# Kernel optimization log

Measured on AMD Instinct MI355X. Metric: run time of the kernel, lower is better.

Reference implementation:

```python
import jax, jax.numpy as jnp
import numpy as np

TOP_K = 2
SCALING = 16.0 / 8.0  # alpha / rank


def setup_inputs() -> dict:
    key = jax.random.key(0)
    ks = jax.random.split(key, 9)
    B, V, D, P = 32, 21, 512, 64
    IN, OUT, E, R, H = D * P, 96, 8, 8, 256
    return {
        "x": jax.random.normal(ks[0], (B, V, D, P), jnp.float32),
        "W_base": jax.random.normal(ks[1], (OUT, IN), jnp.float32) * (IN ** -0.5),
        "b_base": jax.random.normal(ks[2], (OUT,), jnp.float32) * 0.01,
        "W1": jax.random.normal(ks[3], (H, D), jnp.float32) * (D ** -0.5),
        "b1": jax.random.normal(ks[4], (H,), jnp.float32) * 0.01,
        "W2": jax.random.normal(ks[5], (E, H), jnp.float32) * (H ** -0.5),
        "b2": jax.random.normal(ks[6], (E,), jnp.float32) * 0.01,
        "lora_A": jax.random.normal(ks[7], (E, R, IN), jnp.float32) * (IN ** -0.5),
        "lora_B": jax.random.normal(ks[8], (E, OUT, R), jnp.float32) * (R ** -0.5),
    }


def reference(x, W_base, b_base, W1, b1, W2, b2, lora_A, lora_B):
    B, V, D, P = x.shape
    E = lora_A.shape[0]
    # FlattenHead: flatten last two dims, then linear (dropout is identity in eval)
    flat = x.reshape(B, V, D * P)                      # [B, V, IN]
    base_out = flat @ W_base.T + b_base                # [B, V, OUT]
    # Router: pool over n_vars then patch dim -> [B, D]
    pooled = x.mean(axis=1).mean(axis=-1)
    h = jax.nn.relu(pooled @ W1.T + b1)
    logits = h @ W2.T + b2                             # [B, E]
    probs = jax.nn.softmax(logits, axis=-1)
    topw, topi = jax.lax.top_k(probs, TOP_K)           # [B, K]
    topw = topw / jnp.clip(topw.sum(-1, keepdims=True), 1e-6)
    # All LoRA experts (matches original dense compute), then weighted combine
    temp = jnp.einsum("bvi,eri->ebvr", flat, lora_A)   # [E, B, V, R]
    delta = jnp.einsum("ebvr,eor->ebvo", temp, lora_B) * SCALING  # [E, B, V, OUT]
    # Scatter top-k weights into dense [B, E] then combine (top-k sparse combine)
    w_full = jnp.zeros((B, E), x.dtype).at[jnp.arange(B)[:, None], topi].add(topw)
    moe_delta = jnp.einsum("be,ebvo->bvo", w_full, delta)
    return base_out + moe_delta, probs
```

## Files before the change

kernel.cpp:

```cpp
#include <hip/hip_runtime.h>

#define B_DIM 32
#define V_DIM 21
#define D_DIM 512
#define P_DIM 64
#define M_TOTAL 672
#define K_TOTAL 32768
#define OUT_DIM 96
#define E_DIM 8
#define R_DIM 8
#define H_DIM 256
#define N_TOTAL 160
#define SCALING 2.0f
#define POOL_SCALE (1.0f / (V_DIM * (float)P_DIM))

#define BM 64
#define BK 32
#define KSPLIT 32
#define K_PER_SPLIT (K_TOTAL / KSPLIT)
#define CHUNKS (K_PER_SPLIT / BK)
#define SMN (M_TOTAL * N_TOTAL)
#define NMB 11
#define RC_ROWS 4

typedef __attribute__((ext_vector_type(4))) float floatx4;
typedef __attribute__((ext_vector_type(8))) short short8;
typedef __attribute__((ext_vector_type(2))) unsigned int uintx2;

__device__ __forceinline__ unsigned int cvt_pk_bf16(float lo, float hi) {
  unsigned int r;
  asm("v_cvt_pk_bf16_f32 %0, %1, %2" : "=v"(r) : "v"(lo), "v"(hi));
  return r;
}

__device__ __forceinline__ void gl_lds16(const void* g, void* l) {
  __builtin_amdgcn_global_load_lds(
      (const __attribute__((address_space(1))) void*)g,
      (__attribute__((address_space(3))) void*)l, 16, 0, 0);
}

__global__ __launch_bounds__(256, 4)
void gemm_kernel(const float* __restrict__ x, const float* __restrict__ W_base,
                 const float* __restrict__ lora_A, float* __restrict__ P,
                 float* __restrict__ pp) {
  __shared__ __attribute__((aligned(16))) float ldsA[2][BM * BK];
  __shared__ __attribute__((aligned(16))) short ldsB[2][N_TOTAL * BK];
  __shared__ float lds_pool[5 * 16];

  const int tid = threadIdx.x;
  const int mb = blockIdx.x;
  const int m0 = mb * BM;
  const int ky = blockIdx.y;
  const int kbase = ky * K_PER_SPLIT;
  const int lane = tid & 63;
  const int wave = tid >> 6;
  const int quad = lane >> 4;
  const int l16 = lane & 15;
  const int b_first = m0 / V_DIM;
  const int d_first = ky * (K_PER_SPLIT / P_DIM);

  if (tid < 80) lds_pool[tid] = 0.0f;

  const float* srcA[2]; int dstA[2];
  #pragma unroll
  for (int it = 0; it < 2; ++it) {
    int idx = it * 256 + tid;
    int row = idx >> 3, j = idx & 7;
    int m = m0 + row; if (m > M_TOTAL - 1) m = M_TOTAL - 1;
    srcA[it] = x + (size_t)m * K_TOTAL + kbase + ((j ^ (row & 7)) << 2);
    dstA[it] = (it * 256 + (tid & 192)) << 2;
  }

  const float* srcB[5]; int offB[5];
  #pragma unroll
  for (int it = 0; it < 5; ++it) {
    int idx = it * 256 + tid;
    int row = idx >> 3, j = idx & 7;
    const float* wrow = (row < OUT_DIM)
        ? (W_base + (size_t)row * K_TOTAL)
        : (lora_A + (size_t)(row - OUT_DIM) * K_TOTAL);
    srcB[it] = wrow + kbase + (j << 2);
    int p = row >> 1;
    int c8 = ((row & 1) << 2) | (j >> 1);
    offB[it] = p * 64 + ((c8 ^ (p & 7)) << 3) + ((j & 1) << 2);
  }

  const int prow = tid >> 2;
  const int part = tid & 3;
  const int ps1 = (prow + part) & 7;
  const int ps2 = (ps1 + 4) & 7;
  const int pm = m0 + prow;
  const int pool_base = (pm < M_TOTAL) ? ((pm / V_DIM) - b_first) * 16 : -1;

  floatx4 rb[5];
  floatx4 acc[10];
  #pragma unroll
  for (int nt = 0; nt < 10; ++nt) acc[nt] = (floatx4)(0.0f);

#define BLOAD(c)                                                              \
  { _Pragma("unroll")                                                         \
    for (int it = 0; it < 5; ++it)                                            \
      rb[it] = *(const floatx4*)(srcB[it] + (c) * BK); }
#define AISSUE(c, bb)                                                         \
  { _Pragma("unroll")                                                         \
    for (int it = 0; it < 2; ++it)                                            \
      gl_lds16(srcA[it] + (c) * BK, &ldsA[bb][dstA[it]]); }
#define BWRITE(bb)                                                            \
  { _Pragma("unroll")                                                         \
    for (int it = 0; it < 5; ++it) {                                          \
      uintx2 w;                                                               \
      w[0] = cvt_pk_bf16(rb[it][0], rb[it][1]);                               \
      w[1] = cvt_pk_bf16(rb[it][2], rb[it][3]);                               \
      *(uintx2*)&ldsB[bb][offB[it]] = w;                                      \
    } }

  BLOAD(0); AISSUE(0, 0); BWRITE(0);
  __syncthreads();

  #pragma unroll 2
  for (int c = 0; c < CHUNKS; ++c) {
    const int buf = c & 1;
    if (c + 1 < CHUNKS) { BLOAD(c + 1); AISSUE(c + 1, buf ^ 1); }
    {
      const floatx4* aT = (const floatx4*)ldsA[buf];
      floatx4 u = aT[prow * 8 + ps1];
      floatx4 w = aT[prow * 8 + ps2];
      float s = ((u[0] + u[1]) + (u[2] + u[3])) + ((w[0] + w[1]) + (w[2] + w[3]));
      s += __shfl_down(s, 2, 4);
      s += __shfl_down(s, 1, 4);
      if (part == 0 && pool_base >= 0)
        atomicAdd(&lds_pool[pool_base + (c >> 1)], s);
    }
    {
      const floatx4* aT = (const floatx4*)ldsA[buf];
      const int r = wave * 16 + l16;
      floatx4 f0 = aT[r * 8 + ((2 * quad) ^ (r & 7))];
      floatx4 f1 = aT[r * 8 + ((2 * quad + 1) ^ (r & 7))];
      union { short8 s; unsigned int u[4]; } av;
      av.u[0] = cvt_pk_bf16(f0[0], f0[1]);
      av.u[1] = cvt_pk_bf16(f0[2], f0[3]);
      av.u[2] = cvt_pk_bf16(f1[0], f1[1]);
      av.u[3] = cvt_pk_bf16(f1[2], f1[3]);
      const short8* bT = (const short8*)ldsB[buf];
      #pragma unroll
      for (int nt = 0; nt < 10; ++nt) {
        int r2 = nt * 16 + l16;
        int pr = r2 >> 1;
        short8 b = bT[pr * 8 + ((((r2 & 1) << 2) | quad) ^ (pr & 7))];
        acc[nt] = __builtin_amdgcn_mfma_f32_16x16x32_bf16(av.s, b, acc[nt], 0, 0, 0);
      }
    }
    if (c + 1 < CHUNKS) BWRITE(buf ^ 1);
    __syncthreads();
  }

  {
    const int mrow = m0 + wave * 16 + quad * 4;
    float* Pp = P + (size_t)ky * SMN + (size_t)mrow * N_TOTAL + l16;
    #pragma unroll
    for (int r = 0; r < 4; ++r)
      if (mrow + r < M_TOTAL)
        #pragma unroll
        for (int nt = 0; nt < 10; ++nt)
          Pp[(size_t)r * N_TOTAL + nt * 16] = acc[nt][r];
  }

  if (tid < 80) {
    int bl = tid >> 4, dl = tid & 15;
    pp[((size_t)(mb * 5 + bl)) * D_DIM + d_first + dl] = lds_pool[tid];
  }
}

__global__ __launch_bounds__(256)
void router_kernel(const float* __restrict__ pp, const float* __restrict__ W1,
                   const float* __restrict__ b1, const float* __restrict__ W2,
                   const float* __restrict__ b2, float* __restrict__ wfull,
                   float* __restrict__ probs_out) {
  __shared__ float sp[D_DIM];
  __shared__ float sh[H_DIM];
  __shared__ float slog[E_DIM];
  const int b = blockIdx.x;
  const int t = threadIdx.x;
  const int mb1 = (b * V_DIM) / BM;
  const int mb2 = (b * V_DIM + V_DIM - 1) / BM;
  const int bf1 = (mb1 * BM) / V_DIM;
  const int bf2 = (mb2 * BM) / V_DIM;
  const float* p1 = pp + (size_t)(mb1 * 5 + (b - bf1)) * D_DIM;
  const float* p2 = pp + (size_t)(mb2 * 5 + (b - bf2)) * D_DIM;
  for (int d = t; d < D_DIM; d += 256) {
    float v = p1[d];
    if (mb2 != mb1) v += p2[d];
    sp[d] = v * POOL_SCALE;
  }
  __syncthreads();
  float acc = b1[t];
  const float* w1r = W1 + (size_t)t * D_DIM;
  for (int d = 0; d < D_DIM; ++d) acc += sp[d] * w1r[d];
  sh[t] = fmaxf(acc, 0.0f);
  __syncthreads();
  if (t < E_DIM) {
    float a = b2[t];
    const float* w2r = W2 + t * H_DIM;
    for (int j = 0; j < H_DIM; ++j) a += sh[j] * w2r[j];
    slog[t] = a;
  }
  __syncthreads();
  if (t == 0) {
    float p[E_DIM];
    float mx = slog[0];
    for (int e = 1; e < E_DIM; ++e) mx = fmaxf(mx, slog[e]);
    float se = 0.0f;
    for (int e = 0; e < E_DIM; ++e) { p[e] = __expf(slog[e] - mx); se += p[e]; }
    float inv = 1.0f / se;
    for (int e = 0; e < E_DIM; ++e) { p[e] *= inv; probs_out[b * E_DIM + e] = p[e]; }
    int i0 = 0;
    for (int e = 1; e < E_DIM; ++e) if (p[e] > p[i0]) i0 = e;
    int i1 = (i0 == 0) ? 1 : 0;
    for (int e = 0; e < E_DIM; ++e) if (e != i0 && p[e] > p[i1]) i1 = e;
    float s2 = p[i0] + p[i1];
    float invs = 1.0f / fmaxf(s2, 1e-6f);
    for (int e = 0; e < E_DIM; ++e) {
      float w = 0.0f;
      if (e == i0) w += p[i0] * invs;
      if (e == i1) w += p[i1] * invs;
      wfull[b * E_DIM + e] = w;
    }
  }
}

__global__ __launch_bounds__(256)
void reduce_combine_kernel(const float* __restrict__ P, const float* __restrict__ b_base,
                           const float* __restrict__ lora_B, const float* __restrict__ wfull,
                           float* __restrict__ out) {
  __shared__ float sS[RC_ROWS * N_TOTAL];
  const int t = threadIdx.x;
  const int NF4 = RC_ROWS * N_TOTAL / 4;
  if (t < NF4) {
    const floatx4* P4 = (const floatx4*)P;
    size_t base = (size_t)blockIdx.x * NF4 + t;
    floatx4 a = (floatx4)(0.0f);
    #pragma unroll 8
    for (int k = 0; k < KSPLIT; ++k) a += P4[(size_t)k * (SMN / 4) + base];
    *(floatx4*)&sS[t * 4] = a;
  }
  __syncthreads();
  for (int i = t; i < RC_ROWS * OUT_DIM; i += 256) {
    int mr = i / OUT_DIM;
    int o = i - mr * OUT_DIM;
    int mm = blockIdx.x * RC_ROWS + mr;
    int b = mm / V_DIM;
    const float* srow = sS + mr * N_TOTAL;
    float res = srow[o] + b_base[o];
    float moe = 0.0f;
    #pragma unroll
    for (int e = 0; e < E_DIM; ++e) {
      float we = wfull[b * E_DIM + e];
      if (we != 0.0f) {
        const float* lb = lora_B + ((size_t)e * OUT_DIM + o) * R_DIM;
        float dd = 0.0f;
        #pragma unroll
        for (int r = 0; r < R_DIM; ++r) dd += srow[OUT_DIM + e * R_DIM + r] * lb[r];
        moe += we * dd;
      }
    }
    out[(size_t)mm * OUT_DIM + o] = res + SCALING * moe;
  }
}

extern "C" void kernel_launch(void* const* d_in, const int* in_sizes, int n_in,
                              void* d_out, int out_size, void* d_ws, size_t ws_size,
                              hipStream_t stream) {
  const float* x      = (const float*)d_in[0];
  const float* W_base = (const float*)d_in[1];
  const float* b_base = (const float*)d_in[2];
  const float* W1     = (const float*)d_in[3];
  const float* b1     = (const float*)d_in[4];
  const float* W2     = (const float*)d_in[5];
  const float* b2     = (const float*)d_in[6];
  const float* lora_A = (const float*)d_in[7];
  const float* lora_B = (const float*)d_in[8];
  float* out = (float*)d_out;

  float* ws    = (float*)d_ws;
  float* pp    = ws;
  float* wfull = ws + NMB * 5 * D_DIM;
  float* P     = wfull + 256;

  gemm_kernel<<<dim3(NMB, KSPLIT), 256, 0, stream>>>(x, W_base, lora_A, P, pp);
  router_kernel<<<B_DIM, 256, 0, stream>>>(pp, W1, b1, W2, b2, wfull,
                                           out + (size_t)M_TOTAL * OUT_DIM);
  reduce_combine_kernel<<<M_TOTAL / RC_ROWS, 256, 0, stream>>>(
      P, b_base, lora_B, wfull, out);
}
```

Measured before the change: 216.9 us.

## Pre-convert weights to bf16 and use 4-stage async LDS pipeline

```diff
diff --git a/kernel.cpp b/kernel.cpp
--- a/kernel.cpp
+++ b/kernel.cpp
@@ -25,7 +25,12 @@
 
 typedef __attribute__((ext_vector_type(4))) float floatx4;
 typedef __attribute__((ext_vector_type(8))) short short8;
-typedef __attribute__((ext_vector_type(2))) unsigned int uintx2;
+
+__device__ __forceinline__ unsigned short f2bf(float f) {
+  union { float f; unsigned int u; } v; v.f = f;
+  unsigned int u = v.u + (0x7FFFu + ((v.u >> 16) & 1u));
+  return (unsigned short)(u >> 16);
+}
 
 __device__ __forceinline__ unsigned int cvt_pk_bf16(float lo, float hi) {
   unsigned int r;
@@ -39,12 +44,30 @@
       (__attribute__((address_space(3))) void*)l, 16, 0, 0);
 }
 
-__global__ __launch_bounds__(256, 4)
-void gemm_kernel(const float* __restrict__ x, const float* __restrict__ W_base,
-                 const float* __restrict__ lora_A, float* __restrict__ P,
-                 float* __restrict__ pp) {
-  __shared__ __attribute__((aligned(16))) float ldsA[2][BM * BK];
-  __shared__ __attribute__((aligned(16))) short ldsB[2][N_TOTAL * BK];
+__global__ __launch_bounds__(256)
+void convW_kernel(const float* __restrict__ W_base, const float* __restrict__ lora_A,
+                  short* __restrict__ Wb) {
+  int gid = blockIdx.x * 256 + threadIdx.x;
+  size_t base = (size_t)gid * 8;
+  int row = (int)(base >> 15);
+  int k = (int)(base & 32767);
+  const float* src = (row < OUT_DIM) ? (W_base + ((size_t)row << 15) + k)
+                                     : (lora_A + ((size_t)(row - OUT_DIM) << 15) + k);
+  floatx4 v0 = ((const floatx4*)src)[0];
+  floatx4 v1 = ((const floatx4*)src)[1];
+  short8 sv;
+  sv[0] = (short)f2bf(v0[0]); sv[1] = (short)f2bf(v0[1]);
+  sv[2] = (short)f2bf(v0[2]); sv[3] = (short)f2bf(v0[3]);
+  sv[4] = (short)f2bf(v1[0]); sv[5] = (short)f2bf(v1[1]);
+  sv[6] = (short)f2bf(v1[2]); sv[7] = (short)f2bf(v1[3]);
+  *(short8*)(Wb + base) = sv;
+}
+
+__global__ __launch_bounds__(256, 2)
+void gemm_kernel(const float* __restrict__ x, const short* __restrict__ Wb,
+                 float* __restrict__ P, float* __restrict__ pp) {
+  __shared__ __attribute__((aligned(16))) float ldsA[4][BM * BK];
+  __shared__ __attribute__((aligned(16))) short ldsB[4][N_TOTAL * BK];
   __shared__ float lds_pool[5 * 16];
 
   const int tid = threadIdx.x;
@@ -70,19 +93,19 @@
     srcA[it] = x + (size_t)m * K_TOTAL + kbase + ((j ^ (row & 7)) << 2);
     dstA[it] = (it * 256 + (tid & 192)) << 2;
   }
-
-  const float* srcB[5]; int offB[5];
+  const short* srcB[3]; int dstB[3];
   #pragma unroll
-  for (int it = 0; it < 5; ++it) {
+  for (int it = 0; it < 3; ++it) {
     int idx = it * 256 + tid;
-    int row = idx >> 3, j = idx & 7;
-    const float* wrow = (row < OUT_DIM)
-        ? (W_base + (size_t)row * K_TOTAL)
-        : (lora_A + (size_t)(row - OUT_DIM) * K_TOTAL);
-    srcB[it] = wrow + kbase + (j << 2);
-    int p = row >> 1;
-    int c8 = ((row & 1) << 2) | (j >> 1);
-    offB[it] = p * 64 + ((c8 ^ (p & 7)) << 3) + ((j & 1) << 2);
+    if (idx < 640) {
+      int pair = idx >> 3, s8 = idx & 7;
+      int c8 = s8 ^ (pair & 7);
+      int row = pair * 2 + (c8 >> 2), j = c8 & 3;
+      srcB[it] = Wb + (size_t)row * K_TOTAL + kbase + (j << 3);
+      dstB[it] = (it * 256 + (tid & 192)) << 3;
+    } else {
+      srcB[it] = Wb; dstB[it] = 0;
+    }
   }
 
   const int prow = tid >> 2;
@@ -92,35 +115,38 @@
   const int pm = m0 + prow;
   const int pool_base = (pm < M_TOTAL) ? ((pm / V_DIM) - b_first) * 16 : -1;
 
-  floatx4 rb[5];
+#define ISSUE(c, bb)                                                          \
+  {                                                                           \
+    _Pragma("unroll")                                                         \
+    for (int it = 0; it < 2; ++it)                                            \
+      gl_lds16(srcA[it] + (c) * BK, &ldsA[bb][dstA[it]]);                     \
+    _Pragma("unroll")                                                         \
+    for (int it = 0; it < 2; ++it)                                            \
+      gl_lds16(srcB[it] + (c) * BK, &ldsB[bb][dstB[it]]);                     \
+    if (tid < 128) gl_lds16(srcB[2] + (c) * BK, &ldsB[bb][dstB[2]]);          \
+  }
+
   floatx4 acc[10];
   #pragma unroll
   for (int nt = 0; nt < 10; ++nt) acc[nt] = (floatx4)(0.0f);
 
-#define BLOAD(c)                                                              \
-  { _Pragma("unroll")                                                         \
-    for (int it = 0; it < 5; ++it)                                            \
-      rb[it] = *(const floatx4*)(srcB[it] + (c) * BK); }
-#define AISSUE(c, bb)                                                         \
-  { _Pragma("unroll")                                                         \
-    for (int it = 0; it < 2; ++it)                                            \
-      gl_lds16(srcA[it] + (c) * BK, &ldsA[bb][dstA[it]]); }
-#define BWRITE(bb)                                                            \
-  { _Pragma("unroll")                                                         \
-    for (int it = 0; it < 5; ++it) {                                          \
-      uintx2 w;                                                               \
-      w[0] = cvt_pk_bf16(rb[it][0], rb[it][1]);                               \
-      w[1] = cvt_pk_bf16(rb[it][2], rb[it][3]);                               \
-      *(uintx2*)&ldsB[bb][offB[it]] = w;                                      \
-    } }
-
-  BLOAD(0); AISSUE(0, 0); BWRITE(0);
-  __syncthreads();
-
-  #pragma unroll 2
+  ISSUE(0, 0);
+  ISSUE(1, 1);
+  asm volatile("s_waitcnt lgkmcnt(0)" ::: "memory");
+
+  #pragma unroll 4
   for (int c = 0; c < CHUNKS; ++c) {
-    const int buf = c & 1;
-    if (c + 1 < CHUNKS) { BLOAD(c + 1); AISSUE(c + 1, buf ^ 1); }
+    const int buf = c & 3;
+    if (c + 1 < CHUNKS) {
+      if (wave < 2) asm volatile("s_waitcnt vmcnt(5)" ::: "memory");
+      else          asm volatile("s_waitcnt vmcnt(4)" ::: "memory");
+    } else {
+      asm volatile("s_waitcnt vmcnt(0)" ::: "memory");
+    }
+    __builtin_amdgcn_sched_barrier(0);
+    __builtin_amdgcn_s_barrier();
+    __builtin_amdgcn_sched_barrier(0);
+    if (c + 2 < CHUNKS) ISSUE(c + 2, (c + 2) & 3);
     {
       const floatx4* aT = (const floatx4*)ldsA[buf];
       floatx4 u = aT[prow * 8 + ps1];
@@ -150,9 +176,9 @@
         acc[nt] = __builtin_amdgcn_mfma_f32_16x16x32_bf16(av.s, b, acc[nt], 0, 0, 0);
       }
     }
-    if (c + 1 < CHUNKS) BWRITE(buf ^ 1);
-    __syncthreads();
-  }
+  }
+
+  __syncthreads();
 
   {
     const int mrow = m0 + wave * 16 + quad * 4;
@@ -284,9 +310,12 @@
   float* ws    = (float*)d_ws;
   float* pp    = ws;
   float* wfull = ws + NMB * 5 * D_DIM;
-  float* P     = wfull + 256;
-
-  gemm_kernel<<<dim3(NMB, KSPLIT), 256, 0, stream>>>(x, W_base, lora_A, P, pp);
+  short* Wb    = (short*)(wfull + 256);
+  float* P     = (float*)(Wb + (size_t)N_TOTAL * K_TOTAL);
+
+  convW_kernel<<<(N_TOTAL * K_TOTAL / 8 + 255) / 256, 256, 0, stream>>>(
+      W_base, lora_A, Wb);
+  gemm_kernel<<<dim3(NMB, KSPLIT), 256, 0, stream>>>(x, Wb, P, pp);
   router_kernel<<<B_DIM, 256, 0, stream>>>(pp, W1, b1, W2, b2, wfull,
                                            out + (size_t)M_TOTAL * OUT_DIM);
   reduce_combine_kernel<<<M_TOTAL / RC_ROWS, 256, 0, stream>>>(
```

Result: no change. 215.4 us (-0.7%).
